# Kernel tuning notes

Measured on AMD Instinct MI355X. Metric: run time of the kernel, lower is better.

## Reference

```python
import jax, jax.numpy as jnp
import numpy as np

N, D, H, E = 8192, 1024, 4096, 8


def setup_inputs() -> dict:
    key = jax.random.key(0)
    ks = jax.random.split(key, 5)
    s_in = 1.0 / np.sqrt(D)
    s_h = 1.0 / np.sqrt(H)
    return {
        "x": jax.random.normal(ks[0], (N, D), dtype=jnp.float32),
        "Wg": jax.random.normal(ks[1], (D, E), dtype=jnp.float32) * s_in,
        "bg": jnp.zeros((E,), dtype=jnp.float32),
        "W1": jax.random.normal(ks[2], (E, D, H), dtype=jnp.float32) * s_in,
        "b1": jnp.zeros((E, H), dtype=jnp.float32),
        "W2": jax.random.normal(ks[3], (E, H, D), dtype=jnp.float32) * s_h,
        "b2": jnp.zeros((E, D), dtype=jnp.float32),
    }


def reference(x, Wg, bg, W1, b1, W2, b2):
    # gate: softmax linear router -> weights [N, E]
    weights = jax.nn.softmax(x @ Wg + bg, axis=-1)
    # all experts, batched GEMMs: h [N, E, H]
    h = jax.nn.relu(jnp.einsum("nd,edh->neh", x, W1) + b1)  # Dropout is identity at inference
    outputs = jnp.einsum("neh,ehd->ned", h, W2) + b2         # [N, E, D]
    # weighted combine over experts
    return jnp.einsum("ne,ned->nd", weights, outputs)
```

## Files before the change

### kernel.cpp

```cpp
#include <hip/hip_runtime.h>
#include <hip/hip_bf16.h>

#define DDIM 1024
#define HDIM 4096
#define NEXP 8
#define NROW 8192
#define KPAIR 8192

typedef __attribute__((ext_vector_type(8))) short s16x8;
typedef __attribute__((ext_vector_type(4))) float f32x4;

using bf16 = __hip_bfloat16;

__device__ __forceinline__ void gload16(const bf16* g, bf16* lds) {
    __builtin_amdgcn_global_load_lds(
        (const __attribute__((address_space(1))) unsigned int*)g,
        (__attribute__((address_space(3))) unsigned int*)lds,
        16, 0, 0);
}

template <int N>
__device__ __forceinline__ void wait_vmcnt() {
    if constexpr (N == 6)      asm volatile("s_waitcnt vmcnt(6)" ::: "memory");
    else if constexpr (N == 3) asm volatile("s_waitcnt vmcnt(3)" ::: "memory");
    else                       asm volatile("s_waitcnt vmcnt(0)" ::: "memory");
}

__global__ void cvt_x_kernel(const float* __restrict__ x, bf16* __restrict__ xb, int total4) {
    int i = blockIdx.x * 256 + threadIdx.x;
    if (i >= total4) return;
    float4 v = ((const float4*)x)[i];
    union { bf16 b[4]; uint2 u; } p;
    p.b[0] = __float2bfloat16(v.x);
    p.b[1] = __float2bfloat16(v.y);
    p.b[2] = __float2bfloat16(v.z);
    p.b[3] = __float2bfloat16(v.w);
    ((uint2*)xb)[i] = p.u;
}

__global__ void transpose_cvt_kernel(const float* __restrict__ src, bf16* __restrict__ dst,
                                     int R, int C, int ldo, size_t szs, int dzo) {
    __shared__ float t[128][65];
    const float* s = src + (size_t)blockIdx.z * szs;
    bf16* d = dst + (size_t)blockIdx.z * dzo;
    const int r0 = blockIdx.y * 64, c0 = blockIdx.x * 128;
    const int tid = threadIdx.x;
    const int lrow = tid >> 5, lc4 = tid & 31;
#pragma unroll
    for (int i = 0; i < 8; ++i) {
        int rr = i * 8 + lrow;
        float4 v = *(const float4*)&s[(size_t)(r0 + rr) * C + c0 + lc4 * 4];
        t[lc4 * 4 + 0][rr] = v.x;
        t[lc4 * 4 + 1][rr] = v.y;
        t[lc4 * 4 + 2][rr] = v.z;
        t[lc4 * 4 + 3][rr] = v.w;
    }
    __syncthreads();
    const int oc = tid >> 3, oj = tid & 7;
#pragma unroll
    for (int i = 0; i < 4; ++i) {
        int c = oc + i * 32;
        union { bf16 b[8]; s16x8 v; } p;
#pragma unroll
        for (int q = 0; q < 8; ++q) p.b[q] = __float2bfloat16(t[c][oj * 8 + q]);
        *(s16x8*)&d[(size_t)(c0 + c) * ldo + r0 + oj * 8] = p.v;
    }
}

__global__ void gate_kernel(const float* __restrict__ x, const float* __restrict__ Wg,
                            const float* __restrict__ bg, float* __restrict__ wts) {
    int wave = threadIdx.x >> 6, lane = threadIdx.x & 63;
    int n = blockIdx.x * 4 + wave;
    const float* xr = x + (size_t)n * DDIM;
    float acc[NEXP] = {0.f, 0.f, 0.f, 0.f, 0.f, 0.f, 0.f, 0.f};
    for (int d = lane; d < DDIM; d += 64) {
        float xv = xr[d];
        const float* wr = Wg + (size_t)d * NEXP;
#pragma unroll
        for (int e = 0; e < NEXP; ++e) acc[e] += xv * wr[e];
    }
#pragma unroll
    for (int off = 32; off > 0; off >>= 1) {
#pragma unroll
        for (int e = 0; e < NEXP; ++e) acc[e] += __shfl_xor(acc[e], off, 64);
    }
    if (lane == 0) {
        float mx = -1e30f;
#pragma unroll
        for (int e = 0; e < NEXP; ++e) { acc[e] += bg[e]; mx = fmaxf(mx, acc[e]); }
        float s = 0.f;
#pragma unroll
        for (int e = 0; e < NEXP; ++e) { acc[e] = __expf(acc[e] - mx); s += acc[e]; }
        float inv = 1.0f / s;
#pragma unroll
        for (int e = 0; e < NEXP; ++e) wts[(size_t)n * NEXP + e] = acc[e] * inv;
    }
}

__global__ void out_init_kernel(const float* __restrict__ wts, const float* __restrict__ b2,
                                float* __restrict__ out) {
    size_t idx = (size_t)blockIdx.x * 256 + threadIdx.x;
    int d = (int)(idx & (DDIM - 1));
    size_t n = idx >> 10;
    const float* w = wts + n * NEXP;
    float s = 0.f;
#pragma unroll
    for (int e = 0; e < NEXP; ++e) s += w[e] * b2[(size_t)e * DDIM + d];
    out[idx] = s;
}

__global__ __launch_bounds__(512, 1) void gemm1(
    const bf16* __restrict__ A, const bf16* __restrict__ BT, bf16* __restrict__ Cout,
    const float* __restrict__ bias, const float* __restrict__ wts,
    int lda, int ldb, int ldc, int NT, int tilesM, int tilesN, int XGN, int expert) {
    constexpr int WROWS = 128;
    constexpr int HALFA = 256 * 32;
    constexpr int HALFB = 256 * 32;
    constexpr int ATOT = 2 * HALFA;
    constexpr int BUFE = ATOT + 2 * HALFB;
    __shared__ __align__(16) bf16 smem[2 * BUFE];

    const int tid = threadIdx.x;
    const int wave = tid >> 6, lane = tid & 63;
    const int wm = wave >> 2, wn = wave & 3;
    const int r = lane & 15, kg = lane >> 4;

    const int xcd = blockIdx.x & 7, slot = blockIdx.x >> 3;
    const int XGM = 8 / XGN;
    const int rm = tilesM / XGM, rn = tilesN / XGN;
    const int g = slot >> 5, u = slot & 31;
    const int gpr = rn >> 3;
    const int gm = (g / gpr) * 4 + (u >> 3);
    const int gn = (g % gpr) * 8 + (u & 7);
    const int tm = (xcd / XGN) * rm + gm;
    const int tn = (xcd % XGN) * rn + gn;

    const bf16* gA = A + (size_t)tm * 256 * lda;
    const bf16* gB = BT + (size_t)tn * 256 * ldb;

    f32x4 acc[8][4];
#pragma unroll
    for (int m = 0; m < 8; ++m)
#pragma unroll
        for (int n = 0; n < 4; ++n) acc[m][n] = (f32x4){0.f, 0.f, 0.f, 0.f};

    auto stageA = [&](int t, int ks) {
        bf16* dst = smem + (t & 1) * BUFE + ks * HALFA;
#pragma unroll
        for (int j = 0; j < 2; ++j) {
            int c = j * 512 + tid;
            int R = c >> 2, kc = (c & 3) ^ ((R >> 1) & 3);
            gload16(gA + (size_t)R * lda + t * 64 + ks * 32 + kc * 8,
                    dst + (j * 512 + wave * 64) * 8);
        }
    };
    auto stageB = [&](int t, int ks) {
        bf16* dst = smem + (t & 1) * BUFE + ATOT + ks * HALFB;
#pragma unroll
        for (int j = 0; j < 2; ++j) {
            int c = j * 512 + tid;
            int R = c >> 2, kc = (c & 3) ^ ((R >> 1) & 3);
            gload16(gB + (size_t)R * ldb + t * 64 + ks * 32 + kc * 8,
                    dst + (j * 512 + wave * 64) * 8);
        }
    };

    s16x8 a0[4], bb[4];
    auto ldA = [&](int buf, int ks, int mh) {
#pragma unroll
        for (int m = 0; m < 4; ++m) {
            int R = wm * WROWS + mh * 64 + m * 16 + r;
            a0[m] = *(const s16x8*)&smem[buf * BUFE + ks * HALFA + R * 32 +
                                         ((kg ^ ((R >> 1) & 3)) * 8)];
        }
    };
    auto ldB = [&](int buf, int ks) {
#pragma unroll
        for (int n = 0; n < 4; ++n) {
            int R = wn * 64 + n * 16 + r;
            bb[n] = *(const s16x8*)&smem[buf * BUFE + ATOT + ks * HALFB + R * 32 +
                                         ((kg ^ ((R >> 1) & 3)) * 8)];
        }
    };

    auto preMFMA = [&]() {
        __builtin_amdgcn_s_barrier();
        asm volatile("s_waitcnt lgkmcnt(0)" ::: "memory");
        __builtin_amdgcn_sched_barrier(0);
        __builtin_amdgcn_s_setprio(1);
    };
    auto postMFMA = [&](bool vm) {
        __builtin_amdgcn_s_setprio(0);
        if (vm) wait_vmcnt<6>();
        __builtin_amdgcn_s_barrier();
    };
    auto mfmaLo = [&]() {
#pragma unroll
        for (int m = 0; m < 4; ++m)
#pragma unroll
            for (int n = 0; n < 4; ++n)
                acc[m][n] = __builtin_amdgcn_mfma_f32_16x16x32_bf16(a0[m], bb[n], acc[m][n], 0, 0, 0);
    };
    auto mfmaHi = [&]() {
#pragma unroll
        for (int m = 0; m < 4; ++m)
#pragma unroll
            for (int n = 0; n < 4; ++n)
                acc[4 + m][n] = __builtin_amdgcn_mfma_f32_16x16x32_bf16(a0[m], bb[n], acc[4 + m][n], 0, 0, 0);
    };

    stageB(0, 0); stageA(0, 0); stageB(0, 1); stageA(0, 1);
    stageB(1, 0); stageA(1, 0); stageB(1, 1);
    wait_vmcnt<6>();
    __builtin_amdgcn_s_barrier();

    const int NI = NT / 2;
    for (int i = 0; i < NI; ++i) {
        const int t0 = 2 * i, t1 = t0 + 1;
        const bool g2 = (t0 + 2 < NT), g3 = (t1 + 2 < NT);
        ldB(0, 0); ldA(0, 0, 0); stageA(t1, 1);
        preMFMA(); mfmaLo(); postMFMA(false);
        ldA(0, 0, 1); if (g2) stageB(t0 + 2, 0);
        preMFMA(); mfmaHi(); postMFMA(false);
        ldB(0, 1); ldA(0, 1, 0); if (g2) stageA(t0 + 2, 0);
        preMFMA(); mfmaLo(); postMFMA(false);
        ldA(0, 1, 1); if (g2) stageB(t0 + 2, 1);
        preMFMA(); mfmaHi(); postMFMA(true);
        ldB(1, 0); ldA(1, 0, 0); if (g2) stageA(t0 + 2, 1);
        preMFMA(); mfmaLo(); postMFMA(false);
        ldA(1, 0, 1); if (g3) stageB(t1 + 2, 0);
        preMFMA(); mfmaHi(); postMFMA(false);
        ldB(1, 1); ldA(1, 1, 0); if (g3) stageA(t1 + 2, 0);
        preMFMA(); mfmaLo(); postMFMA(false);
        ldA(1, 1, 1); if (g3) stageB(t1 + 2, 1);
        preMFMA(); mfmaHi(); postMFMA(true);
    }

    bf16* hs = smem;
    const int col0 = tn * 256 + wn * 64;
#pragma unroll
    for (int n = 0; n < 4; ++n) {
        float bv = bias[col0 + n * 16 + r];
        int cl = wn * 64 + n * 16 + r;
#pragma unroll
        for (int mf = 0; mf < 8; ++mf) {
#pragma unroll
            for (int j = 0; j < 4; ++j) {
                int rl = wm * WROWS + (mf >> 2) * 64 + (mf & 3) * 16 + kg * 4 + j;
                float wv = wts[((size_t)tm * 256 + rl) * NEXP + expert];
                float v = acc[mf][n][j] + bv;
                v = v > 0.f ? v : 0.f;
                hs[rl * 256 + cl] = __float2bfloat16(wv * v);
            }
        }
    }
    __builtin_amdgcn_s_barrier();
    asm volatile("s_waitcnt lgkmcnt(0)" ::: "memory");
    const size_t rbase = (size_t)tm * 256;
    const int cbase = tn * 256;
#pragma unroll
    for (int i2 = 0; i2 < 16; ++i2) {
        int rl = wave * 32 + i2 * 2 + (lane >> 5);
        int c8 = (lane & 31) * 8;
        s16x8 v = *(const s16x8*)&hs[rl * 256 + c8];
        *(s16x8*)&Cout[(rbase + rl) * (size_t)ldc + cbase + c8] = v;
    }
}

__global__ __launch_bounds__(512, 1) void gemm2pair(
    const bf16* __restrict__ A, const bf16* __restrict__ BT, float* __restrict__ O,
    int lda, int ldb, int ldc, int NT, int tilesM, int tilesN, int XGN) {
    constexpr int HALFA = 256 * 32;
    constexpr int HALFB = 128 * 32;
    constexpr int ATOT = 2 * HALFA;
    constexpr int BUFE = ATOT + 2 * HALFB;
    constexpr int RSTR = 68;
    __shared__ __align__(16) bf16 smem[3 * BUFE];

    const int tid = threadIdx.x;
    const int wave = tid >> 6, lane = tid & 63;
    const int ksw = wave & 1, wn = (wave >> 1) & 1, wm = wave >> 2;
    const int r = lane & 15, kg = lane >> 4;

    const int xcd = blockIdx.x & 7, slot = blockIdx.x >> 3;
    const int XGM = 8 / XGN;
    const int rm = tilesM / XGM, rn = tilesN / XGN;
    const int g = slot >> 5, u = slot & 31;
    const int gpr = rn >> 3;
    const int gm = (g / gpr) * 4 + (u >> 3);
    const int gn = (g % gpr) * 8 + (u & 7);
    const int tm = (xcd / XGN) * rm + gm;
    const int tn = (xcd % XGN) * rn + gn;

    const bf16* gA = A + (size_t)tm * 256 * lda;
    const bf16* gB = BT + (size_t)tn * 128 * ldb;

    f32x4 acc[8][4];
#pragma unroll
    for (int m = 0; m < 8; ++m)
#pragma unroll
        for (int n = 0; n < 4; ++n) acc[m][n] = (f32x4){0.f, 0.f, 0.f, 0.f};

    auto stageA = [&](int t, int ks) {
        bf16* dst = smem + (t % 3) * BUFE + ks * HALFA;
#pragma unroll
        for (int j = 0; j < 2; ++j) {
            int c = j * 512 + tid;
            int R = c >> 2, kc = (c & 3) ^ ((R >> 1) & 3);
            gload16(gA + (size_t)R * lda + t * 64 + ks * 32 + kc * 8,
                    dst + (j * 512 + wave * 64) * 8);
        }
    };
    auto stageB = [&](int t, int ks) {
        bf16* dst = smem + (t % 3) * BUFE + ATOT + ks * HALFB;
        int R = tid >> 2, kc = (tid & 3) ^ ((R >> 1) & 3);
        gload16(gB + (size_t)R * ldb + t * 64 + ks * 32 + kc * 8, dst + (wave * 64) * 8);
    };

    s16x8 a0[4], a1[4], bfr[4];
    auto ldA0 = [&](int rb) {
#pragma unroll
        for (int m = 0; m < 4; ++m) {
            int R = wm * 128 + m * 16 + r;
            a0[m] = *(const s16x8*)&smem[rb * BUFE + ksw * HALFA + R * 32 +
                                         ((kg ^ ((R >> 1) & 3)) * 8)];
        }
    };
    auto ldA1 = [&](int rb) {
#pragma unroll
        for (int m = 0; m < 4; ++m) {
            int R = wm * 128 + 64 + m * 16 + r;
            a1[m] = *(const s16x8*)&smem[rb * BUFE + ksw * HALFA + R * 32 +
                                         ((kg ^ ((R >> 1) & 3)) * 8)];
        }
    };
    auto ldB = [&](int rb) {
#pragma unroll
        for (int n = 0; n < 4; ++n) {
            int R = wn * 64 + n * 16 + r;
            bfr[n] = *(const s16x8*)&smem[rb * BUFE + ATOT + ksw * HALFB + R * 32 +
                                          ((kg ^ ((R >> 1) & 3)) * 8)];
        }
    };

    stageA(0, 0); stageB(0, 0); stageA(0, 1); stageB(0, 1);
    stageA(1, 0); stageB(1, 0); stageA(1, 1); stageB(1, 1);
    wait_vmcnt<6>();
    __builtin_amdgcn_s_barrier();

    for (int t = 0; t < NT; ++t) {
        const int rb = t % 3;
        const bool gg = (t + 2 < NT);
        ldB(rb); ldA0(rb);
        if (gg) { stageA(t + 2, 0); stageB(t + 2, 0); }
        ldA1(rb);
        if (gg) { stageA(t + 2, 1); stageB(t + 2, 1); }
        asm volatile("s_waitcnt lgkmcnt(4)" ::: "memory");
        __builtin_amdgcn_sched_barrier(0);
        __builtin_amdgcn_s_setprio(1);
#pragma unroll
        for (int m = 0; m < 4; ++m)
#pragma unroll
            for (int n = 0; n < 4; ++n)
                acc[m][n] = __builtin_amdgcn_mfma_f32_16x16x32_bf16(a0[m], bfr[n], acc[m][n], 0, 0, 0);
        __builtin_amdgcn_s_setprio(0);
        asm volatile("s_waitcnt lgkmcnt(0)" ::: "memory");
        __builtin_amdgcn_sched_barrier(0);
        __builtin_amdgcn_s_setprio(1);
#pragma unroll
        for (int m = 0; m < 4; ++m)
#pragma unroll
            for (int n = 0; n < 4; ++n)
                acc[4 + m][n] = __builtin_amdgcn_mfma_f32_16x16x32_bf16(a1[m], bfr[n], acc[4 + m][n], 0, 0, 0);
        __builtin_amdgcn_s_setprio(0);
        if (t + 1 < NT) {
            if (gg) wait_vmcnt<6>();
            else    wait_vmcnt<0>();
            __builtin_amdgcn_s_barrier();
        }
    }

    __syncthreads();
    float* red = (float*)smem;
    const int zone = (wm * 2 + wn) * (128 * RSTR);
    if (ksw == 1) {
#pragma unroll
        for (int mf = 0; mf < 8; ++mf) {
#pragma unroll
            for (int n = 0; n < 4; ++n) {
                int rl = (mf >> 2) * 64 + (mf & 3) * 16 + kg * 4;
                int cl = n * 16 + r;
#pragma unroll
                for (int j = 0; j < 4; ++j)
                    red[zone + (rl + j) * RSTR + cl] = acc[mf][n][j];
            }
        }
    }
    __syncthreads();
    if (ksw == 0) {
        const size_t row0 = (size_t)tm * 256 + wm * 128;
        const int col0 = tn * 128 + wn * 64;
#pragma unroll
        for (int mf = 0; mf < 8; ++mf) {
#pragma unroll
            for (int j = 0; j < 4; ++j) {
                int rl = (mf >> 2) * 64 + (mf & 3) * 16 + kg * 4 + j;
                size_t rr = row0 + rl;
#pragma unroll
                for (int n = 0; n < 4; ++n) {
                    int cl = n * 16 + r;
                    float v = acc[mf][n][j] + red[zone + rl * RSTR + cl];
                    O[rr * (size_t)ldc + col0 + cl] += v;
                }
            }
        }
    }
}

extern "C" void kernel_launch(void* const* d_in, const int* in_sizes, int n_in,
                              void* d_out, int out_size, void* d_ws, size_t ws_size,
                              hipStream_t stream) {
    const float* x  = (const float*)d_in[0];
    const float* Wg = (const float*)d_in[1];
    const float* bg = (const float*)d_in[2];
    const float* W1 = (const float*)d_in[3];
    const float* b1 = (const float*)d_in[4];
    const float* W2 = (const float*)d_in[5];
    const float* b2 = (const float*)d_in[6];
    float* out = (float*)d_out;

    char* ws = (char*)d_ws;
    bf16* xb   = (bf16*)(ws);
    bf16* W1Te = (bf16*)(ws + (16ull << 20));
    bf16* W2P  = (bf16*)(ws + (24ull << 20));
    bf16* Hs   = (bf16*)(ws + (40ull << 20));
    float* wts = (float*)(ws + (168ull << 20));

    cvt_x_kernel<<<NROW * DDIM / 4 / 256, 256, 0, stream>>>(x, xb, NROW * DDIM / 4);
    gate_kernel<<<NROW / 4, 256, 0, stream>>>(x, Wg, bg, wts);
    out_init_kernel<<<NROW * DDIM / 256, 256, 0, stream>>>(wts, b2, out);

    for (int p = 0; p < 4; ++p) {
        for (int h = 0; h < 2; ++h) {
            int e = 2 * p + h;
            transpose_cvt_kernel<<<dim3(HDIM / 128, DDIM / 64, 1), 256, 0, stream>>>(
                W1 + (size_t)e * DDIM * HDIM, W1Te, DDIM, HDIM, DDIM, 0, 0);
            gemm1<<<512, 512, 0, stream>>>(
                xb, W1Te, Hs + (size_t)h * HDIM, b1 + (size_t)e * HDIM, wts,
                DDIM, DDIM, KPAIR, DDIM / 64, 32, 16, 2, e);
        }
        transpose_cvt_kernel<<<dim3(DDIM / 128, HDIM / 64, 2), 256, 0, stream>>>(
            W2 + (size_t)2 * p * HDIM * DDIM, W2P, HDIM, DDIM, KPAIR,
            (size_t)HDIM * DDIM, HDIM);
        gemm2pair<<<256, 512, 0, stream>>>(
            Hs, W2P, out, KPAIR, KPAIR, DDIM, KPAIR / 64, 32, 8, 1);
    }
}
```

Baseline: 1.310 ms.

## Fuse x conversion with gating and batch expert pairs into single gemm1 launches

Merges the bf16 conversion of x with the gate softmax kernel, so x is read once and one launch is dropped. It also transposes both experts' W1 in one launch and runs gemm1 over both experts with a doubled grid, where the block index selects the expert. This cuts the launch count and the gaps between small kernels, and gives each gemm1 launch more blocks to fill the GPU. The cost is a larger workspace for the paired W1, and the tile-to-XCD mapping now spans two experts.

```diff
diff --git a/kernel.cpp b/kernel.cpp
--- a/kernel.cpp
+++ b/kernel.cpp
@@ -26,16 +26,46 @@
     else                       asm volatile("s_waitcnt vmcnt(0)" ::: "memory");
 }
 
-__global__ void cvt_x_kernel(const float* __restrict__ x, bf16* __restrict__ xb, int total4) {
-    int i = blockIdx.x * 256 + threadIdx.x;
-    if (i >= total4) return;
-    float4 v = ((const float4*)x)[i];
-    union { bf16 b[4]; uint2 u; } p;
-    p.b[0] = __float2bfloat16(v.x);
-    p.b[1] = __float2bfloat16(v.y);
-    p.b[2] = __float2bfloat16(v.z);
-    p.b[3] = __float2bfloat16(v.w);
-    ((uint2*)xb)[i] = p.u;
+__global__ void cvtgate_kernel(const float* __restrict__ x, const float* __restrict__ Wg,
+                               const float* __restrict__ bg, bf16* __restrict__ xb,
+                               float* __restrict__ wts) {
+    int wave = threadIdx.x >> 6, lane = threadIdx.x & 63;
+    int n = blockIdx.x * 4 + wave;
+    const float* xr = x + (size_t)n * DDIM;
+    bf16* xbr = xb + (size_t)n * DDIM;
+    float acc[NEXP] = {0.f, 0.f, 0.f, 0.f, 0.f, 0.f, 0.f, 0.f};
+#pragma unroll
+    for (int j = 0; j < 4; ++j) {
+        int d0 = j * 256 + lane * 4;
+        float4 v = *(const float4*)&xr[d0];
+        union { bf16 b[4]; uint2 u; } pk;
+        pk.b[0] = __float2bfloat16(v.x);
+        pk.b[1] = __float2bfloat16(v.y);
+        pk.b[2] = __float2bfloat16(v.z);
+        pk.b[3] = __float2bfloat16(v.w);
+        *(uint2*)&xbr[d0] = pk.u;
+        const float* w0 = Wg + (size_t)d0 * NEXP;
+#pragma unroll
+        for (int e = 0; e < NEXP; ++e)
+            acc[e] += v.x * w0[e] + v.y * w0[NEXP + e] + v.z * w0[2 * NEXP + e] +
+                      v.w * w0[3 * NEXP + e];
+    }
+#pragma unroll
+    for (int off = 32; off > 0; off >>= 1) {
+#pragma unroll
+        for (int e = 0; e < NEXP; ++e) acc[e] += __shfl_xor(acc[e], off, 64);
+    }
+    if (lane == 0) {
+        float mx = -1e30f;
+#pragma unroll
+        for (int e = 0; e < NEXP; ++e) { acc[e] += bg[e]; mx = fmaxf(mx, acc[e]); }
+        float s = 0.f;
+#pragma unroll
+        for (int e = 0; e < NEXP; ++e) { acc[e] = __expf(acc[e] - mx); s += acc[e]; }
+        float inv = 1.0f / s;
+#pragma unroll
+        for (int e = 0; e < NEXP; ++e) wts[(size_t)n * NEXP + e] = acc[e] * inv;
+    }
 }
 
 __global__ void transpose_cvt_kernel(const float* __restrict__ src, bf16* __restrict__ dst,
@@ -67,36 +97,6 @@
     }
 }
 
-__global__ void gate_kernel(const float* __restrict__ x, const float* __restrict__ Wg,
-                            const float* __restrict__ bg, float* __restrict__ wts) {
-    int wave = threadIdx.x >> 6, lane = threadIdx.x & 63;
-    int n = blockIdx.x * 4 + wave;
-    const float* xr = x + (size_t)n * DDIM;
-    float acc[NEXP] = {0.f, 0.f, 0.f, 0.f, 0.f, 0.f, 0.f, 0.f};
-    for (int d = lane; d < DDIM; d += 64) {
-        float xv = xr[d];
-        const float* wr = Wg + (size_t)d * NEXP;
-#pragma unroll
-        for (int e = 0; e < NEXP; ++e) acc[e] += xv * wr[e];
-    }
-#pragma unroll
-    for (int off = 32; off > 0; off >>= 1) {
-#pragma unroll
-        for (int e = 0; e < NEXP; ++e) acc[e] += __shfl_xor(acc[e], off, 64);
-    }
-    if (lane == 0) {
-        float mx = -1e30f;
-#pragma unroll
-        for (int e = 0; e < NEXP; ++e) { acc[e] += bg[e]; mx = fmaxf(mx, acc[e]); }
-        float s = 0.f;
-#pragma unroll
-        for (int e = 0; e < NEXP; ++e) { acc[e] = __expf(acc[e] - mx); s += acc[e]; }
-        float inv = 1.0f / s;
-#pragma unroll
-        for (int e = 0; e < NEXP; ++e) wts[(size_t)n * NEXP + e] = acc[e] * inv;
-    }
-}
-
 __global__ void out_init_kernel(const float* __restrict__ wts, const float* __restrict__ b2,
                                 float* __restrict__ out) {
     size_t idx = (size_t)blockIdx.x * 256 + threadIdx.x;
@@ -110,9 +110,9 @@
 }
 
 __global__ __launch_bounds__(512, 1) void gemm1(
-    const bf16* __restrict__ A, const bf16* __restrict__ BT, bf16* __restrict__ Cout,
-    const float* __restrict__ bias, const float* __restrict__ wts,
-    int lda, int ldb, int ldc, int NT, int tilesM, int tilesN, int XGN, int expert) {
+    const bf16* __restrict__ A, const bf16* __restrict__ BTp, bf16* __restrict__ Hsb,
+    const float* __restrict__ b1p, const float* __restrict__ wts,
+    int lda, int ldb, int ldc, int NT, int tilesM, int tilesN, int XGN, int e0) {
     constexpr int WROWS = 128;
     constexpr int HALFA = 256 * 32;
     constexpr int HALFB = 256 * 32;
@@ -125,7 +125,14 @@
     const int wm = wave >> 2, wn = wave & 3;
     const int r = lane & 15, kg = lane >> 4;
 
-    const int xcd = blockIdx.x & 7, slot = blockIdx.x >> 3;
+    const int eh = blockIdx.x >> 9;
+    const int bx = blockIdx.x & 511;
+    const bf16* BT = BTp + (size_t)eh * HDIM * DDIM;
+    bf16* Cout = Hsb + (size_t)eh * HDIM;
+    const float* bias = b1p + (size_t)eh * HDIM;
+    const int expert = e0 + eh;
+
+    const int xcd = bx & 7, slot = bx >> 3;
     const int XGM = 8 / XGN;
     const int rm = tilesM / XGM, rn = tilesN / XGN;
     const int g = slot >> 5, u = slot & 31;
@@ -431,24 +438,21 @@
 
     char* ws = (char*)d_ws;
     bf16* xb   = (bf16*)(ws);
-    bf16* W1Te = (bf16*)(ws + (16ull << 20));
-    bf16* W2P  = (bf16*)(ws + (24ull << 20));
-    bf16* Hs   = (bf16*)(ws + (40ull << 20));
-    float* wts = (float*)(ws + (168ull << 20));
-
-    cvt_x_kernel<<<NROW * DDIM / 4 / 256, 256, 0, stream>>>(x, xb, NROW * DDIM / 4);
-    gate_kernel<<<NROW / 4, 256, 0, stream>>>(x, Wg, bg, wts);
+    bf16* W1P  = (bf16*)(ws + (16ull << 20));
+    bf16* W2P  = (bf16*)(ws + (32ull << 20));
+    bf16* Hs   = (bf16*)(ws + (48ull << 20));
+    float* wts = (float*)(ws + (176ull << 20));
+
+    cvtgate_kernel<<<NROW / 4, 256, 0, stream>>>(x, Wg, bg, xb, wts);
     out_init_kernel<<<NROW * DDIM / 256, 256, 0, stream>>>(wts, b2, out);
 
     for (int p = 0; p < 4; ++p) {
-        for (int h = 0; h < 2; ++h) {
-            int e = 2 * p + h;
-            transpose_cvt_kernel<<<dim3(HDIM / 128, DDIM / 64, 1), 256, 0, stream>>>(
-                W1 + (size_t)e * DDIM * HDIM, W1Te, DDIM, HDIM, DDIM, 0, 0);
-            gemm1<<<512, 512, 0, stream>>>(
-                xb, W1Te, Hs + (size_t)h * HDIM, b1 + (size_t)e * HDIM, wts,
-                DDIM, DDIM, KPAIR, DDIM / 64, 32, 16, 2, e);
-        }
+        transpose_cvt_kernel<<<dim3(HDIM / 128, DDIM / 64, 2), 256, 0, stream>>>(
+            W1 + (size_t)2 * p * DDIM * HDIM, W1P, DDIM, HDIM, DDIM,
+            (size_t)DDIM * HDIM, HDIM * DDIM);
+        gemm1<<<1024, 512, 0, stream>>>(
+            xb, W1P, Hs, b1 + (size_t)2 * p * HDIM, wts,
+            DDIM, DDIM, KPAIR, DDIM / 64, 32, 16, 2, 2 * p);
         transpose_cvt_kernel<<<dim3(DDIM / 128, HDIM / 64, 2), 256, 0, stream>>>(
             W2 + (size_t)2 * p * HDIM * DDIM, W2P, HDIM, DDIM, KPAIR,
             (size_t)HDIM * DDIM, HDIM);
```

Result: no change. 1.297 ms (-1.0%).
